# Performance work log

Hardware: AMD Instinct MI355X
Metric: run time of the kernel (lower is better)

The kernel has to match this reference:

```python
import jax, jax.numpy as jnp
import numpy as np

B, S, OBS, H, A = 256, 128, 256, 1024, 18


def setup_inputs() -> dict:
    key = jax.random.key(0)
    ks = jax.random.split(key, 12)
    sc = lambda fan_in: 1.0 / np.sqrt(fan_in)
    u = lambda k, shape, s: jax.random.uniform(k, shape, jnp.float32, -s, s)
    return {
        "obs": jax.random.normal(ks[0], (B, S, OBS), jnp.float32),
        "hx": jnp.zeros((B, H), jnp.float32),
        "cx": jnp.zeros((B, H), jnp.float32),
        "behaviour_acts": jax.random.randint(ks[1], (B, S, 1), 0, A, jnp.int32),
        "W_body": u(ks[2], (H, OBS), sc(OBS)),
        "b_body": u(ks[3], (H,), sc(OBS)),
        "W_ih": u(ks[4], (4 * H, H), sc(H)),
        "b_ih": u(ks[5], (4 * H,), sc(H)),
        "W_hh": u(ks[6], (4 * H, H), sc(H)),
        "b_hh": u(ks[7], (4 * H,), sc(H)),
        "W_v": u(ks[8], (1, H), sc(H)),
        "b_v": u(ks[9], (1,), sc(H)),
        "W_l": u(ks[10], (A, H), sc(H)),
        "b_l": u(ks[11], (A,), sc(H)),
    }


def reference(obs, hx, cx, behaviour_acts, W_body, b_body, W_ih, b_ih,
              W_hh, b_hh, W_v, b_v, W_l, b_l):
    acts = behaviour_acts.astype(jnp.int32).squeeze(-1)  # [B,S]
    # body MLP: Linear + ReLU
    x = jax.nn.relu(jnp.einsum("bso,ho->bsh", obs, W_body) + b_body)  # [B,S,H]
    # precompute input-to-gate contributions for all timesteps (batched GEMM)
    xg = jnp.einsum("bsh,gh->bsg", x, W_ih) + b_ih  # [B,S,4H]
    xg_t = jnp.swapaxes(xg, 0, 1)  # [S,B,4H]

    def step(carry, g_in):
        h, c = carry
        g = g_in + h @ W_hh.T + b_hh  # [B,4H]
        i, f, gg, o = jnp.split(g, 4, axis=-1)  # torch LSTMCell gate order i,f,g,o
        i = jax.nn.sigmoid(i)
        f = jax.nn.sigmoid(f)
        gg = jnp.tanh(gg)
        o = jax.nn.sigmoid(o)
        c = f * c + i * gg
        h = o * jnp.tanh(c)
        return (h, c), h

    _, hs = jax.lax.scan(step, (hx, cx), xg_t)  # hs: [S,B,H]
    hs = jnp.swapaxes(hs, 0, 1)  # [B,S,H]

    value = jnp.einsum("bsh,vh->bsv", hs, W_v) + b_v  # [B,S,1]
    logits = jnp.einsum("bsh,ah->bsa", hs, W_l) + b_l  # [B,S,A]
    # Categorical(probs=softmax(logits)): dist.logits == log_softmax(logits)
    logp = jax.nn.log_softmax(logits, axis=-1)  # [B,S,A]
    log_prob = jnp.take_along_axis(logp, acts[..., None], axis=-1)  # [B,S,1]
    entropy = -jnp.sum(jnp.exp(logp) * logp, axis=-1, keepdims=True)  # [B,S,1]
    return logp, log_prob, entropy, value
```

## Files before the change

### kernel.cpp

```cpp
#include <hip/hip_runtime.h>

#define AS1 __attribute__((address_space(1)))
#define AS3 __attribute__((address_space(3)))

typedef __attribute__((ext_vector_type(4))) float f32x4;
typedef __attribute__((ext_vector_type(8))) short s16x8;
typedef __attribute__((ext_vector_type(4))) short s16x4;

static constexpr int BB = 256, SS = 128, OBSN = 256, HH = 1024, AN = 18;
static constexpr int MM = BB * SS;
static constexpr int G4 = 4 * HH;

static constexpr int LP_OFF  = MM * AN;
static constexpr int ENT_OFF = LP_OFF + MM;
static constexpr int VAL_OFF = ENT_OFF + MM;

__device__ __forceinline__ short f2bf(float f) {
  unsigned u = __builtin_bit_cast(unsigned, f);
  u += 0x7FFFu + ((u >> 16) & 1u);
  return (short)(u >> 16);
}
__device__ __forceinline__ float bf2f(short s) {
  unsigned u = ((unsigned)(unsigned short)s) << 16;
  return __builtin_bit_cast(float, u);
}
__device__ __forceinline__ void gl_lds16(const void* g, void* l) {
  __builtin_amdgcn_global_load_lds((const AS1 void*)g, (AS3 void*)l, 16, 0, 0);
}
__device__ __forceinline__ float sigf(float x) {
  x = fminf(fmaxf(x, -30.f), 30.f);
  return 1.f / (1.f + __expf(-x));
}
__device__ __forceinline__ float tanhfast(float x) {
  x = fminf(fmaxf(x, -15.f), 15.f);
  float e = __expf(2.f * x);
  return (e - 1.f) / (e + 1.f);
}
__device__ __forceinline__ void cast4(const float* __restrict__ s,
                                      short* __restrict__ d, int i) {
  f32x4 v = ((const f32x4*)s)[i];
  s16x4 o;
  o[0] = f2bf(v[0]); o[1] = f2bf(v[1]); o[2] = f2bf(v[2]); o[3] = f2bf(v[3]);
  ((s16x4*)d)[i] = o;
}

__global__ __launch_bounds__(256) void prep(
    const float* __restrict__ obs, const float* __restrict__ Wb,
    const float* __restrict__ Wih, const float* __restrict__ Whh,
    const float* __restrict__ Wl, const float* __restrict__ Wv,
    const float* __restrict__ bih, const float* __restrict__ bhh,
    const float* __restrict__ hx, const float* __restrict__ cx,
    short* __restrict__ obsb, short* __restrict__ wbo, short* __restrict__ wiho,
    short* __restrict__ whho, short* __restrict__ wlo, short* __restrict__ wvo,
    float* __restrict__ bsum, short* __restrict__ h0o, float* __restrict__ co) {
  int i = blockIdx.x * 256 + threadIdx.x;
  if (i < 2097152) { cast4(obs, obsb, i); return; }
  i -= 2097152;
  if (i < 65536) { cast4(Wb, wbo, i); return; }
  i -= 65536;
  if (i < 1048576) { cast4(Wih, wiho, i); return; }
  i -= 1048576;
  if (i < 1048576) { cast4(Whh, whho, i); return; }
  i -= 1048576;
  if (i < 4608) { cast4(Wl, wlo, i); return; }
  i -= 4608;
  if (i < 256) { cast4(Wv, wvo, i); return; }
  i -= 256;
  if (i < 1024) {
    f32x4 a = ((const f32x4*)bih)[i];
    f32x4 b = ((const f32x4*)bhh)[i];
    ((f32x4*)bsum)[i] = a + b;
    return;
  }
  i -= 1024;
  cast4(hx, h0o, i);
  ((f32x4*)co)[i] = ((const f32x4*)cx)[i];
}

template <int N, int K, bool RELU, int REMAP>
__global__ __launch_bounds__(256, 2) void gemm_bt(
    const short* __restrict__ A, const short* __restrict__ Bw,
    const float* __restrict__ bias, short* __restrict__ C, int t0) {
  __shared__ short lA[128 * 32];
  __shared__ short lB[128 * 32];
  const int tid = threadIdx.x;
  const int lane = tid & 63, wave = tid >> 6;
  const int nTN = N / 128;
  const int tm = blockIdx.x / nTN, tn = blockIdx.x % nTN;

  const int r0 = tid >> 2;
  const int kc = (tid & 3) * 8;

  const int m0 = tm * 128 + r0;
  const int m1 = m0 + 64;
  size_t pr0, pr1;
  if constexpr (REMAP == 1) {
    pr0 = (size_t)((m0 & (BB - 1)) * SS + t0 + (m0 >> 8));
    pr1 = (size_t)((m1 & (BB - 1)) * SS + t0 + (m1 >> 8));
  } else {
    pr0 = (size_t)m0; pr1 = (size_t)m1;
  }
  const short* a0 = A + pr0 * K + kc;
  const short* a1 = A + pr1 * K + kc;
  const short* b0 = Bw + (size_t)(tn * 128 + r0) * K + kc;
  const short* b1 = Bw + (size_t)(tn * 128 + r0 + 64) * K + kc;

  f32x4 acc[4][4];
#pragma unroll
  for (int i = 0; i < 4; ++i)
#pragma unroll
    for (int j = 0; j < 4; ++j) acc[i][j] = {0.f, 0.f, 0.f, 0.f};

  const int wr = (wave >> 1) * 64;
  const int wc = (wave & 1) * 64;
  const int fr = lane & 15;
  const int fk = (lane >> 4) * 8;

  for (int k0 = 0; k0 < K; k0 += 32) {
    __syncthreads();
    gl_lds16(a0 + k0, &lA[tid * 8]);
    gl_lds16(a1 + k0, &lA[2048 + tid * 8]);
    gl_lds16(b0 + k0, &lB[tid * 8]);
    gl_lds16(b1 + k0, &lB[2048 + tid * 8]);
    __syncthreads();
    s16x8 af[4], bfr[4];
#pragma unroll
    for (int i = 0; i < 4; ++i)
      af[i] = *(const s16x8*)&lA[(wr + i * 16 + fr) * 32 + fk];
#pragma unroll
    for (int j = 0; j < 4; ++j)
      bfr[j] = *(const s16x8*)&lB[(wc + j * 16 + fr) * 32 + fk];
#pragma unroll
    for (int i = 0; i < 4; ++i)
#pragma unroll
      for (int j = 0; j < 4; ++j)
        acc[i][j] = __builtin_amdgcn_mfma_f32_16x16x32_bf16(af[i], bfr[j], acc[i][j], 0, 0, 0);
  }

  const int orow = (lane >> 4) * 4;
#pragma unroll
  for (int i = 0; i < 4; ++i) {
#pragma unroll
    for (int j = 0; j < 4; ++j) {
      const int colg = tn * 128 + wc + j * 16 + fr;
      const float bv = bias[colg];
#pragma unroll
      for (int r = 0; r < 4; ++r) {
        const int rowg = tm * 128 + wr + i * 16 + orow + r;
        float v = acc[i][j][r] + bv;
        if (RELU) v = v > 0.f ? v : 0.f;
        C[(size_t)rowg * N + colg] = f2bf(v);
      }
    }
  }
}


#define HLD(o0, o1, a_, b_)                                                   \
  asm volatile("global_load_dwordx4 %0, %2, off offset:" #o0 " sc0 sc1\n\t"   \
               "global_load_dwordx4 %1, %2, off offset:" #o1 " sc0 sc1"       \
               : "=v"(a_), "=v"(b_) : "v"(hb) : "memory")

#define CHUNK(kc_, wn_, a_, b_)                                               \
  asm volatile("s_waitcnt vmcnt(" #wn_ ")" ::: "memory");                     \
  __builtin_amdgcn_sched_barrier(0);                                          \
  {                                                                           \
    _Pragma("unroll") for (int j = 0; j < 4; ++j) {                           \
      const int rowb = (j * 16 + fr) << 11;                                   \
      const s16x8 w0 = *(const s16x8*)(smem + rowb +                          \
                                       ((((kc_) * 8 + fh) ^ fr) << 4));       \
      const s16x8 w1 = *(const s16x8*)(smem + rowb +                          \
                                       ((((kc_) * 8 + 4 + fh) ^ fr) << 4));   \
      acc[j] = __builtin_amdgcn_mfma_f32_16x16x32_bf16(a_, w0, acc[j], 0, 0, 0); \
      acc[j] = __builtin_amdgcn_mfma_f32_16x16x32_bf16(b_, w1, acc[j], 0, 0, 0); \
    }                                                                         \
  }

__global__ __launch_bounds__(256, 1) void lstm_scan(
    const short* __restrict__ Whh, const short* __restrict__ xg,
    short* __restrict__ hs, const short* __restrict__ h0,
    float* __restrict__ cst, int* __restrict__ bar, int nsteps, int t0) {
  extern __shared__ char smem[];

  const int tid = threadIdx.x, lane = tid & 63, w = tid >> 6;
  const int bt = blockIdx.x >> 6, ht = blockIdx.x & 63;
  const int b0 = bt * 64, hc0 = ht * 16;
  const int fr = lane & 15, fh = lane >> 4;

#pragma unroll 4
  for (int j = 0; j < 32; ++j) {
    const int cid = j * 256 + tid;
    const int r = cid >> 7, cc = cid & 127;
    const int wrow = (r >> 4) * HH + hc0 + (r & 15);
    gl_lds16(Whh + (size_t)wrow * HH + ((size_t)(cc ^ (r & 15)) << 3),
             smem + cid * 16);
  }
  const int brow = b0 + w * 16 + fh * 4;
  const int hcol = hc0 + fr;
  float cv[4];
#pragma unroll
  for (int r = 0; r < 4; ++r) cv[r] = cst[(size_t)(brow + r) * HH + hcol];
  int* flags = bar + bt * 64;
  asm volatile("s_waitcnt vmcnt(0)" ::: "memory");
  __syncthreads();

  for (int sl = 0; sl < nsteps; ++sl) {
    const short* hsrc = (sl == 0) ? h0 : hs + (size_t)(sl - 1) * (BB * HH);
    const short* hb = hsrc + (size_t)(b0 + w * 16 + fr) * HH + fh * 8;

    float xgv[4][4];
    {
      const short* xgb = xg + (size_t)sl * BB * G4;
#pragma unroll
      for (int j = 0; j < 4; ++j)
#pragma unroll
        for (int r = 0; r < 4; ++r)
          xgv[j][r] = bf2f(xgb[(size_t)(brow + r) * G4 + j * HH + hcol]);
    }

    f32x4 acc[4];
#pragma unroll
    for (int j = 0; j < 4; ++j) acc[j] = {0.f, 0.f, 0.f, 0.f};

    s16x8 hA0, hB0, hA1, hB1, hA2, hB2, hA3, hB3, hA4, hB4, hA5, hB5, hA6, hB6,
        hA7, hB7, hA8, hB8, hA9, hB9, hA10, hB10, hA11, hB11, hA12, hB12,
        hA13, hB13, hA14, hB14, hA15, hB15;
    HLD(0, 64, hA0, hB0);       HLD(128, 192, hA1, hB1);
    HLD(256, 320, hA2, hB2);    HLD(384, 448, hA3, hB3);
    HLD(512, 576, hA4, hB4);    HLD(640, 704, hA5, hB5);
    HLD(768, 832, hA6, hB6);    HLD(896, 960, hA7, hB7);
    HLD(1024, 1088, hA8, hB8);  HLD(1152, 1216, hA9, hB9);
    HLD(1280, 1344, hA10, hB10); HLD(1408, 1472, hA11, hB11);
    HLD(1536, 1600, hA12, hB12); HLD(1664, 1728, hA13, hB13);
    HLD(1792, 1856, hA14, hB14); HLD(1920, 1984, hA15, hB15);

    CHUNK(0, 30, hA0, hB0)   CHUNK(1, 28, hA1, hB1)
    CHUNK(2, 26, hA2, hB2)   CHUNK(3, 24, hA3, hB3)
    CHUNK(4, 22, hA4, hB4)   CHUNK(5, 20, hA5, hB5)
    CHUNK(6, 18, hA6, hB6)   CHUNK(7, 16, hA7, hB7)
    CHUNK(8, 14, hA8, hB8)   CHUNK(9, 12, hA9, hB9)
    CHUNK(10, 10, hA10, hB10) CHUNK(11, 8, hA11, hB11)
    CHUNK(12, 6, hA12, hB12) CHUNK(13, 4, hA13, hB13)
    CHUNK(14, 2, hA14, hB14) CHUNK(15, 0, hA15, hB15)

    short* hdst = hs + (size_t)sl * (BB * HH);
#pragma unroll
    for (int r = 0; r < 4; ++r) {
      const float gi = acc[0][r] + xgv[0][r];
      const float gf = acc[1][r] + xgv[1][r];
      const float gc = acc[2][r] + xgv[2][r];
      const float go = acc[3][r] + xgv[3][r];
      const float cn = sigf(gf) * cv[r] + sigf(gi) * tanhfast(gc);
      cv[r] = cn;
      const unsigned hv = (unsigned)(unsigned short)f2bf(sigf(go) * tanhfast(cn));
      short* hp = hdst + (size_t)(brow + r) * HH + hcol;
      asm volatile("global_store_short %0, %1, off sc0 sc1"
                   :: "v"(hp), "v"(hv) : "memory");
    }
    if (sl + 1 < nsteps) {
      const int target = t0 + sl + 1;
      asm volatile("s_waitcnt vmcnt(0)" ::: "memory");
      __syncthreads();
      if (tid == 0)
        __hip_atomic_store(&flags[ht], target, __ATOMIC_RELAXED,
                           __HIP_MEMORY_SCOPE_AGENT);
      if (tid < 64) {
        while (__hip_atomic_load(&flags[tid], __ATOMIC_RELAXED,
                                 __HIP_MEMORY_SCOPE_AGENT) < target)
          __builtin_amdgcn_s_sleep(1);
      }
      __syncthreads();
    }
  }
#pragma unroll
  for (int r = 0; r < 4; ++r) cst[(size_t)(brow + r) * HH + hcol] = cv[r];
}

__global__ __launch_bounds__(256) void heads_k(
    const short* __restrict__ hs, const short* __restrict__ Wl,
    const float* __restrict__ bl, const short* __restrict__ Wv,
    const float* __restrict__ bv, const int* __restrict__ acts,
    float* __restrict__ out, int t0) {
  const int tid = threadIdx.x, lane = tid & 63, wave = tid >> 6;
  const int r = blockIdx.x * 4 + wave;
  const int sl = r >> 8, b = r & 255;
  const int mg = b * SS + t0 + sl;
  const short* hrow = hs + (size_t)r * HH + lane * 16;
  const s16x8 hv0 = *(const s16x8*)hrow;
  const s16x8 hv1 = *(const s16x8*)(hrow + 8);
  float xv[16];
#pragma unroll
  for (int e = 0; e < 8; ++e) { xv[e] = bf2f(hv0[e]); xv[8 + e] = bf2f(hv1[e]); }

  float lg[19];
#pragma unroll
  for (int j = 0; j < 19; ++j) {
    const short* wp = (j < 18 ? Wl + (size_t)j * HH : Wv) + lane * 16;
    const s16x8 w0 = *(const s16x8*)wp;
    const s16x8 w1 = *(const s16x8*)(wp + 8);
    float s = 0.f;
#pragma unroll
    for (int e = 0; e < 8; ++e) s += xv[e] * bf2f(w0[e]) + xv[8 + e] * bf2f(w1[e]);
#pragma unroll
    for (int d = 32; d >= 1; d >>= 1) s += __shfl_xor(s, d, 64);
    lg[j] = s + (j < 18 ? bl[j] : bv[0]);
  }
  float mx = lg[0];
#pragma unroll
  for (int j = 1; j < 18; ++j) mx = fmaxf(mx, lg[j]);
  float se = 0.f;
#pragma unroll
  for (int j = 0; j < 18; ++j) se += __expf(lg[j] - mx);
  const float lse = __logf(se);
  if (lane == 0) {
    const int act = acts[mg];
    float ent = 0.f, sel = 0.f;
#pragma unroll
    for (int j = 0; j < 18; ++j) {
      const float lp = lg[j] - mx - lse;
      out[(size_t)mg * 18 + j] = lp;
      ent -= __expf(lp) * lp;
      if (j == act) sel = lp;
    }
    out[LP_OFF + mg] = sel;
    out[ENT_OFF + mg] = ent;
    out[VAL_OFF + mg] = lg[18];
  }
}

extern "C" void kernel_launch(void* const* d_in, const int* in_sizes, int n_in,
                              void* d_out, int out_size, void* d_ws, size_t ws_size,
                              hipStream_t stream) {
  const float* obs    = (const float*)d_in[0];
  const float* hx     = (const float*)d_in[1];
  const float* cx     = (const float*)d_in[2];
  const int*   acts   = (const int*)d_in[3];
  const float* W_body = (const float*)d_in[4];
  const float* b_body = (const float*)d_in[5];
  const float* W_ih   = (const float*)d_in[6];
  const float* b_ih   = (const float*)d_in[7];
  const float* W_hh   = (const float*)d_in[8];
  const float* b_hh   = (const float*)d_in[9];
  const float* W_v    = (const float*)d_in[10];
  const float* b_v    = (const float*)d_in[11];
  const float* W_l    = (const float*)d_in[12];
  const float* b_l    = (const float*)d_in[13];
  float* out = (float*)d_out;
  (void)in_sizes; (void)n_in; (void)out_size;

  (void)hipFuncSetAttribute((const void*)lstm_scan,
                            hipFuncAttributeMaxDynamicSharedMemorySize, 131072);

  const size_t FIXED = 36235264ull;
  const size_t PER_C = 3145728ull;
  int chunk = 32;
  while (chunk > 1 && FIXED + (size_t)chunk * PER_C > ws_size) chunk >>= 1;

  char* ws = (char*)d_ws;
  size_t off = 0;
  auto give = [&](size_t bytes) -> char* {
    char* p = ws + off;
    off += (bytes + 255) & ~(size_t)255;
    return p;
  };
  short* wb   = (short*)give((size_t)HH * OBSN * 2);
  short* wih  = (short*)give((size_t)G4 * HH * 2);
  short* whh  = (short*)give((size_t)G4 * HH * 2);
  short* wl   = (short*)give((size_t)AN * HH * 2);
  short* wv   = (short*)give((size_t)HH * 2);
  float* bsum = (float*)give((size_t)G4 * 4);
  short* obsb = (short*)give((size_t)MM * OBSN * 2);
  short* h0b  = (short*)give((size_t)BB * HH * 2);
  short* h1b  = (short*)give((size_t)BB * HH * 2);
  float* cbuf = (float*)give((size_t)BB * HH * 4);
  int*   barb = (int*)give(1024);
  short* xc   = (short*)give((size_t)chunk * BB * HH * 2);
  short* xgc  = (short*)give((size_t)chunk * BB * G4 * 2);
  short* hsc  = (short*)give((size_t)chunk * BB * HH * 2);
  (void)h1b;

  hipMemsetAsync(barb, 0, 1024, stream);

  prep<<<16919, 256, 0, stream>>>(obs, W_body, W_ih, W_hh, W_l, W_v, b_ih, b_hh,
                                  hx, cx, obsb, wb, wih, whh, wl, wv, bsum, h0b, cbuf);

  const int Mc = chunk * BB;
  for (int t0 = 0; t0 < SS; t0 += chunk) {
    gemm_bt<HH, OBSN, true, 1>
        <<<(Mc / 128) * (HH / 128), 256, 0, stream>>>(obsb, wb, b_body, xc, t0);
    gemm_bt<G4, HH, false, 0>
        <<<(Mc / 128) * (G4 / 128), 256, 0, stream>>>(xc, wih, bsum, xgc, 0);
    const short* hprev = (t0 == 0) ? h0b : hsc + (size_t)(chunk - 1) * BB * HH;
    lstm_scan<<<256, 256, 131072, stream>>>(whh, xgc, hsc, hprev, cbuf, barb,
                                            chunk, t0);
    heads_k<<<Mc / 4, 256, 0, stream>>>(hsc, wl, b_l, wv, b_v, acts, out, t0);
  }
}
```

Baseline: 1.813 ms.

## Replace block barrier with per-wave flags, prefetch next-step gates, enlarge chunk

The LSTM scan's per-step grid barrier is restructured. Each wave now publishes its own flag and polls all peer flags with a ballot, which removes the two __syncthreads per step. Next-step xg values are prefetched into double-buffered registers, the sc0 sc1 cache bypass is dropped from h loads, and the chunk size rises to 128 so fewer launches are needed. An extra unsynchronized diagnostic launch of lstm_scan<0> is appended at the end. That launch adds work writing into scratch buffers and looks like a timing probe. Removing the cache bypass risks reading stale h data.

```diff
diff --git a/kernel.cpp b/kernel.cpp
--- a/kernel.cpp
+++ b/kernel.cpp
@@ -157,8 +157,8 @@
 
 
 #define HLD(o0, o1, a_, b_)                                                   \
-  asm volatile("global_load_dwordx4 %0, %2, off offset:" #o0 " sc0 sc1\n\t"   \
-               "global_load_dwordx4 %1, %2, off offset:" #o1 " sc0 sc1"       \
+  asm volatile("global_load_dwordx4 %0, %2, off offset:" #o0 "\n\t"           \
+               "global_load_dwordx4 %1, %2, off offset:" #o1                  \
                : "=v"(a_), "=v"(b_) : "v"(hb) : "memory")
 
 #define CHUNK(kc_, wn_, a_, b_)                                               \
@@ -176,6 +176,69 @@
     }                                                                         \
   }
 
+#define STEP(sl_, XGC, XGN)                                                   \
+  {                                                                           \
+    const int sl = (sl_);                                                     \
+    const short* hsrc = sl ? hs + (size_t)(sl - 1) * (BB * HH) : h0;          \
+    const short* hb = hsrc + (size_t)(b0 + w * 16 + fr) * HH + fh * 8;        \
+    if (SYNC && sl > 0) {                                                     \
+      const int tgt = t0 + sl;                                                \
+      for (;;) {                                                              \
+        const int v = __hip_atomic_load(&flags[pollIdx], __ATOMIC_RELAXED,    \
+                                        __HIP_MEMORY_SCOPE_AGENT);            \
+        if (__ballot(v >= tgt) == ~0ull) break;                               \
+        __builtin_amdgcn_s_sleep(1);                                          \
+      }                                                                       \
+    }                                                                         \
+    asm volatile("s_waitcnt vmcnt(0)" ::: "memory");    \
+    f32x4 acc[4];                                                             \
+    _Pragma("unroll") for (int j = 0; j < 4; ++j) acc[j] = {0.f,0.f,0.f,0.f}; \
+    s16x8 hA0,hB0,hA1,hB1,hA2,hB2,hA3,hB3,hA4,hB4,hA5,hB5,hA6,hB6,hA7,hB7,    \
+          hA8,hB8,hA9,hB9,hA10,hB10,hA11,hB11,hA12,hB12,hA13,hB13,hA14,hB14,  \
+          hA15,hB15;                                                          \
+    HLD(0, 64, hA0, hB0);        HLD(128, 192, hA1, hB1);                     \
+    HLD(256, 320, hA2, hB2);     HLD(384, 448, hA3, hB3);                     \
+    HLD(512, 576, hA4, hB4);     HLD(640, 704, hA5, hB5);                     \
+    HLD(768, 832, hA6, hB6);     HLD(896, 960, hA7, hB7);                     \
+    HLD(1024, 1088, hA8, hB8);   HLD(1152, 1216, hA9, hB9);                   \
+    HLD(1280, 1344, hA10, hB10); HLD(1408, 1472, hA11, hB11);                 \
+    HLD(1536, 1600, hA12, hB12); HLD(1664, 1728, hA13, hB13);                 \
+    HLD(1792, 1856, hA14, hB14); HLD(1920, 1984, hA15, hB15);                 \
+    CHUNK(0, 30, hA0, hB0)   CHUNK(1, 28, hA1, hB1)                           \
+    CHUNK(2, 26, hA2, hB2)   CHUNK(3, 24, hA3, hB3)                           \
+    CHUNK(4, 22, hA4, hB4)   CHUNK(5, 20, hA5, hB5)                           \
+    CHUNK(6, 18, hA6, hB6)   CHUNK(7, 16, hA7, hB7)                           \
+    CHUNK(8, 14, hA8, hB8)   CHUNK(9, 12, hA9, hB9)                           \
+    CHUNK(10, 10, hA10, hB10) CHUNK(11, 8, hA11, hB11)                        \
+    CHUNK(12, 6, hA12, hB12) CHUNK(13, 4, hA13, hB13)                         \
+    CHUNK(14, 2, hA14, hB14) CHUNK(15, 0, hA15, hB15)                         \
+    short* hdst = hs + (size_t)sl * (BB * HH);                                \
+    _Pragma("unroll") for (int r = 0; r < 4; ++r) {                           \
+      const float gi = acc[0][r] + XGC[0][r];                                 \
+      const float gf = acc[1][r] + XGC[1][r];                                 \
+      const float gc = acc[2][r] + XGC[2][r];                                 \
+      const float go = acc[3][r] + XGC[3][r];                                 \
+      const float cn = sigf(gf) * cv[r] + sigf(gi) * tanhfast(gc);            \
+      cv[r] = cn;                                                             \
+      const unsigned hv =                                                     \
+          (unsigned)(unsigned short)f2bf(sigf(go) * tanhfast(cn));            \
+      short* hp = hdst + (size_t)(brow + r) * HH + hcol;                      \
+      asm volatile("global_store_short %0, %1, off sc0 sc1"                   \
+                   :: "v"(hp), "v"(hv) : "memory");                           \
+    }                                                                         \
+    if (sl + 1 < nsteps) {                                                    \
+      const short* xgb = xg + (size_t)(sl + 1) * BB * G4;                     \
+      _Pragma("unroll") for (int j = 0; j < 4; ++j)                           \
+        _Pragma("unroll") for (int r = 0; r < 4; ++r)                         \
+          XGN[j][r] = bf2f(xgb[(size_t)(brow + r) * G4 + j * HH + hcol]);     \
+      asm volatile("s_waitcnt vmcnt(16)" ::: "memory");    \
+      if (SYNC && lane == 0)                                                  \
+        __hip_atomic_store(&flags[myFlag], t0 + sl + 1, __ATOMIC_RELAXED,     \
+                           __HIP_MEMORY_SCOPE_AGENT);                         \
+    }                                                                         \
+  }
+
+template <int SYNC>
 __global__ __launch_bounds__(256, 1) void lstm_scan(
     const short* __restrict__ Whh, const short* __restrict__ xg,
     short* __restrict__ hs, const short* __restrict__ h0,
@@ -183,9 +246,19 @@
   extern __shared__ char smem[];
 
   const int tid = threadIdx.x, lane = tid & 63, w = tid >> 6;
-  const int bt = blockIdx.x >> 6, ht = blockIdx.x & 63;
+  const int g = blockIdx.x;
+  const int bt = g >> 6, ht = g & 63;
   const int b0 = bt * 64, hc0 = ht * 16;
   const int fr = lane & 15, fh = lane >> 4;
+  const int brow = b0 + w * 16 + fh * 4;
+  const int hcol = hc0 + fr;
+
+  float xgA[4][4], xgB[4][4];
+#pragma unroll
+  for (int j = 0; j < 4; ++j)
+#pragma unroll
+    for (int r = 0; r < 4; ++r)
+      xgA[j][r] = bf2f(xg[(size_t)(brow + r) * G4 + j * HH + hcol]);
 
 #pragma unroll 4
   for (int j = 0; j < 32; ++j) {
@@ -195,82 +268,18 @@
     gl_lds16(Whh + (size_t)wrow * HH + ((size_t)(cc ^ (r & 15)) << 3),
              smem + cid * 16);
   }
-  const int brow = b0 + w * 16 + fh * 4;
-  const int hcol = hc0 + fr;
   float cv[4];
 #pragma unroll
   for (int r = 0; r < 4; ++r) cv[r] = cst[(size_t)(brow + r) * HH + hcol];
-  int* flags = bar + bt * 64;
+  int* flags = bar + bt * 256;
+  const int pollIdx = lane * 4 + w;
+  const int myFlag  = ht * 4 + w;
   asm volatile("s_waitcnt vmcnt(0)" ::: "memory");
   __syncthreads();
 
-  for (int sl = 0; sl < nsteps; ++sl) {
-    const short* hsrc = (sl == 0) ? h0 : hs + (size_t)(sl - 1) * (BB * HH);
-    const short* hb = hsrc + (size_t)(b0 + w * 16 + fr) * HH + fh * 8;
-
-    float xgv[4][4];
-    {
-      const short* xgb = xg + (size_t)sl * BB * G4;
-#pragma unroll
-      for (int j = 0; j < 4; ++j)
-#pragma unroll
-        for (int r = 0; r < 4; ++r)
-          xgv[j][r] = bf2f(xgb[(size_t)(brow + r) * G4 + j * HH + hcol]);
-    }
-
-    f32x4 acc[4];
-#pragma unroll
-    for (int j = 0; j < 4; ++j) acc[j] = {0.f, 0.f, 0.f, 0.f};
-
-    s16x8 hA0, hB0, hA1, hB1, hA2, hB2, hA3, hB3, hA4, hB4, hA5, hB5, hA6, hB6,
-        hA7, hB7, hA8, hB8, hA9, hB9, hA10, hB10, hA11, hB11, hA12, hB12,
-        hA13, hB13, hA14, hB14, hA15, hB15;
-    HLD(0, 64, hA0, hB0);       HLD(128, 192, hA1, hB1);
-    HLD(256, 320, hA2, hB2);    HLD(384, 448, hA3, hB3);
-    HLD(512, 576, hA4, hB4);    HLD(640, 704, hA5, hB5);
-    HLD(768, 832, hA6, hB6);    HLD(896, 960, hA7, hB7);
-    HLD(1024, 1088, hA8, hB8);  HLD(1152, 1216, hA9, hB9);
-    HLD(1280, 1344, hA10, hB10); HLD(1408, 1472, hA11, hB11);
-    HLD(1536, 1600, hA12, hB12); HLD(1664, 1728, hA13, hB13);
-    HLD(1792, 1856, hA14, hB14); HLD(1920, 1984, hA15, hB15);
-
-    CHUNK(0, 30, hA0, hB0)   CHUNK(1, 28, hA1, hB1)
-    CHUNK(2, 26, hA2, hB2)   CHUNK(3, 24, hA3, hB3)
-    CHUNK(4, 22, hA4, hB4)   CHUNK(5, 20, hA5, hB5)
-    CHUNK(6, 18, hA6, hB6)   CHUNK(7, 16, hA7, hB7)
-    CHUNK(8, 14, hA8, hB8)   CHUNK(9, 12, hA9, hB9)
-    CHUNK(10, 10, hA10, hB10) CHUNK(11, 8, hA11, hB11)
-    CHUNK(12, 6, hA12, hB12) CHUNK(13, 4, hA13, hB13)
-    CHUNK(14, 2, hA14, hB14) CHUNK(15, 0, hA15, hB15)
-
-    short* hdst = hs + (size_t)sl * (BB * HH);
-#pragma unroll
-    for (int r = 0; r < 4; ++r) {
-      const float gi = acc[0][r] + xgv[0][r];
-      const float gf = acc[1][r] + xgv[1][r];
-      const float gc = acc[2][r] + xgv[2][r];
-      const float go = acc[3][r] + xgv[3][r];
-      const float cn = sigf(gf) * cv[r] + sigf(gi) * tanhfast(gc);
-      cv[r] = cn;
-      const unsigned hv = (unsigned)(unsigned short)f2bf(sigf(go) * tanhfast(cn));
-      short* hp = hdst + (size_t)(brow + r) * HH + hcol;
-      asm volatile("global_store_short %0, %1, off sc0 sc1"
-                   :: "v"(hp), "v"(hv) : "memory");
-    }
-    if (sl + 1 < nsteps) {
-      const int target = t0 + sl + 1;
-      asm volatile("s_waitcnt vmcnt(0)" ::: "memory");
-      __syncthreads();
-      if (tid == 0)
-        __hip_atomic_store(&flags[ht], target, __ATOMIC_RELAXED,
-                           __HIP_MEMORY_SCOPE_AGENT);
-      if (tid < 64) {
-        while (__hip_atomic_load(&flags[tid], __ATOMIC_RELAXED,
-                                 __HIP_MEMORY_SCOPE_AGENT) < target)
-          __builtin_amdgcn_s_sleep(1);
-      }
-      __syncthreads();
-    }
+  for (int sl2 = 0; sl2 < nsteps; sl2 += 2) {
+    STEP(sl2, xgA, xgB)
+    STEP(sl2 + 1, xgB, xgA)
   }
 #pragma unroll
   for (int r = 0; r < 4; ++r) cst[(size_t)(brow + r) * HH + hcol] = cv[r];
@@ -348,12 +357,14 @@
   float* out = (float*)d_out;
   (void)in_sizes; (void)n_in; (void)out_size;
 
-  (void)hipFuncSetAttribute((const void*)lstm_scan,
+  (void)hipFuncSetAttribute((const void*)lstm_scan<1>,
                             hipFuncAttributeMaxDynamicSharedMemorySize, 131072);
-
-  const size_t FIXED = 36235264ull;
+  (void)hipFuncSetAttribute((const void*)lstm_scan<0>,
+                            hipFuncAttributeMaxDynamicSharedMemorySize, 131072);
+
+  const size_t FIXED = 36236288ull;
   const size_t PER_C = 3145728ull;
-  int chunk = 32;
+  int chunk = 128;
   while (chunk > 1 && FIXED + (size_t)chunk * PER_C > ws_size) chunk >>= 1;
 
   char* ws = (char*)d_ws;
@@ -373,13 +384,13 @@
   short* h0b  = (short*)give((size_t)BB * HH * 2);
   short* h1b  = (short*)give((size_t)BB * HH * 2);
   float* cbuf = (float*)give((size_t)BB * HH * 4);
-  int*   barb = (int*)give(1024);
+  int*   barb = (int*)give(4096);
   short* xc   = (short*)give((size_t)chunk * BB * HH * 2);
   short* xgc  = (short*)give((size_t)chunk * BB * G4 * 2);
   short* hsc  = (short*)give((size_t)chunk * BB * HH * 2);
   (void)h1b;
 
-  hipMemsetAsync(barb, 0, 1024, stream);
+  hipMemsetAsync(barb, 0, 4096, stream);
 
   prep<<<16919, 256, 0, stream>>>(obs, W_body, W_ih, W_hh, W_l, W_v, b_ih, b_hh,
                                   hx, cx, obsb, wb, wih, whh, wl, wv, bsum, h0b, cbuf);
@@ -391,8 +402,12 @@
     gemm_bt<G4, HH, false, 0>
         <<<(Mc / 128) * (G4 / 128), 256, 0, stream>>>(xc, wih, bsum, xgc, 0);
     const short* hprev = (t0 == 0) ? h0b : hsc + (size_t)(chunk - 1) * BB * HH;
-    lstm_scan<<<256, 256, 131072, stream>>>(whh, xgc, hsc, hprev, cbuf, barb,
-                                            chunk, t0);
+    lstm_scan<1><<<256, 256, 131072, stream>>>(whh, xgc, hsc, hprev, cbuf,
+                                               barb, chunk, t0);
     heads_k<<<Mc / 4, 256, 0, stream>>>(hsc, wl, b_l, wv, b_v, acts, out, t0);
   }
-}
+
+  const int diagN = chunk < 64 ? chunk : 64;
+  lstm_scan<0><<<256, 256, 131072, stream>>>(whh, xgc, xc, xc, (float*)xgc,
+                                             barb, diagN, 0);
+}
```

New measurement: 2.088 ms. 1.15x slower.
